# Kernel tuning notes

Hardware: AMD Instinct MI355X
Metric: run time of the kernel (lower is better)

## Reference

```python
import jax, jax.numpy as jnp
import numpy as np

B, L, DI, D, DO = 64, 1024, 256, 256, 256


def setup_inputs() -> dict:
    key = jax.random.key(0)
    ks = jax.random.split(key, 8)
    s = 1.0 / np.sqrt(D)

    def lin(k, din, dout):
        k1, k2 = jax.random.split(k)
        w = jax.random.normal(k1, (din, dout), dtype=jnp.float32) * s
        b = jax.random.normal(k2, (dout,), dtype=jnp.float32) * s
        return w, b

    Wi_w, Wi_b = lin(ks[0], DI, D)
    Wx_w, Wx_b = lin(ks[1], D, D)
    Ux_w, Ux_b = lin(ks[2], D, D)
    Rx_w, Rx_b = lin(ks[3], D, D)
    Wr_w, Wr_b = lin(ks[4], D, D)
    Wu_w, Wu_b = lin(ks[5], D, D)
    Wo_w, Wo_b = lin(ks[6], D, DO)
    inputs = jax.random.normal(ks[7], (B, L, DI), dtype=jnp.float32)
    return dict(inputs=inputs,
                Wi_w=Wi_w, Wi_b=Wi_b, Wx_w=Wx_w, Wx_b=Wx_b,
                Ux_w=Ux_w, Ux_b=Ux_b, Rx_w=Rx_w, Rx_b=Rx_b,
                Wr_w=Wr_w, Wr_b=Wr_b, Wu_w=Wu_w, Wu_b=Wu_b,
                Wo_w=Wo_w, Wo_b=Wo_b)


def reference(inputs, Wi_w, Wi_b, Wx_w, Wx_b, Ux_w, Ux_b, Rx_w, Rx_b,
              Wr_w, Wr_b, Wu_w, Wu_b, Wo_w, Wo_b):
    x = inputs @ Wi_w + Wi_b  # [B, L, D]

    def run(xd):
        # precompute input projections (one big GEMM each)
        x_x = xd @ Wx_w + Wx_b
        x_r = xd @ Ux_w + Ux_b
        x_u = xd @ Rx_w + Rx_b

        def step(h, xs):
            xx, xr, xu = xs
            r = jax.nn.sigmoid(h @ Wr_w + Wr_b + xr)
            u = jax.nn.sigmoid(h @ Wu_w + Wu_b + xu)
            cand = jnp.tanh(r * h + xx)  # note: module applies r to raw h, no extra matmul
            h_new = u * h + (1.0 - u) * cand
            return h_new, h_new

        h0 = jnp.zeros((xd.shape[0], D), dtype=xd.dtype)
        xs = (jnp.swapaxes(x_x, 0, 1), jnp.swapaxes(x_r, 0, 1), jnp.swapaxes(x_u, 0, 1))
        _, out = jax.lax.scan(step, h0, xs)  # out: [L, B, D]
        return jnp.swapaxes(out, 0, 1)

    out = run(x)
    # bi_gru=True: same weights over time-reversed sequence
    out = out + jnp.flip(run(jnp.flip(x, axis=1)), axis=1)
    return out @ Wo_w + Wo_b
```

## Files before the change

### kernel.cpp

```cpp
#include <hip/hip_runtime.h>


typedef float   f32x4 __attribute__((ext_vector_type(4)));
typedef short   s16x8 __attribute__((ext_vector_type(8)));
typedef int     i32x4 __attribute__((ext_vector_type(4)));
typedef unsigned int u32;
typedef unsigned short u16;

#define LDP  264

__device__ __forceinline__ u16 f2bf(float x) {
    u32 u = __float_as_uint(x);
    return (u16)((u + 0x7FFFu + ((u >> 16) & 1u)) >> 16);
}
__device__ __forceinline__ float bflo(u32 u) { return __uint_as_float(u << 16); }
__device__ __forceinline__ float bfhi(u32 u) { return __uint_as_float(u & 0xFFFF0000u); }
__device__ __forceinline__ float bf2f(u16 v) { return __uint_as_float((u32)v << 16); }

__device__ __forceinline__ float sigm(float z) {
    float e = __builtin_amdgcn_exp2f(z * -1.44269504f);
    return __builtin_amdgcn_rcpf(1.0f + e);
}
__device__ __forceinline__ float tanhfast(float y) {
    float e = __builtin_amdgcn_exp2f(y * 2.88539008f);
    return 1.0f - 2.0f * __builtin_amdgcn_rcpf(1.0f + e);
}

__device__ __forceinline__ void bar_lgkm() {
    asm volatile("s_waitcnt lgkmcnt(0)" ::: "memory");
    __builtin_amdgcn_s_barrier();
    asm volatile("" ::: "memory");
}
__device__ __forceinline__ void bar_only() {
    asm volatile("" ::: "memory");
    __builtin_amdgcn_s_barrier();
    asm volatile("" ::: "memory");
}

#define GLD_LDS16(g, l) __builtin_amdgcn_global_load_lds( \
    (const __attribute__((address_space(1))) unsigned int*)(g), \
    (__attribute__((address_space(3))) unsigned int*)(l), 16, 0, 0)

__global__ __launch_bounds__(256, 2)
void gemm256(const void* __restrict__ Asrc, int a_f32, const u16* __restrict__ A2,
             const float* __restrict__ W, const float* __restrict__ b1,
             const float* __restrict__ b2, void* __restrict__ Cdst, int c_f32, int M)
{
    __shared__ u16 At[32 * LDP];
    const int tid  = threadIdx.x;
    const int lane = tid & 63, wv = tid >> 6;
    const int quad = lane >> 4, n16 = lane & 15;

    s16x8 bw[4][8];
    #pragma unroll
    for (int nt = 0; nt < 4; ++nt) {
        const int col = wv * 64 + nt * 16 + n16;
        #pragma unroll
        for (int kt = 0; kt < 8; ++kt) {
            const int kb0 = kt * 32 + quad * 8;
            s16x8 f;
            #pragma unroll
            for (int j = 0; j < 8; ++j) f[j] = (short)f2bf(W[(kb0 + j) * 256 + col]);
            bw[nt][kt] = f;
        }
    }

    const int arow = tid >> 3, kb = (tid & 7) * 32;
    float av[32];
    const int nstrip = M >> 5;
    const int stride = (int)gridDim.x;

    auto load_strip = [&](int ss) __attribute__((always_inline)) {
        const long base = (long)(ss * 32 + arow) * 256 + kb;
        if (a_f32) {
            const float4* p = (const float4*)((const float*)Asrc + base);
            #pragma unroll
            for (int i = 0; i < 8; ++i) {
                float4 v = p[i];
                av[i*4+0] = v.x; av[i*4+1] = v.y; av[i*4+2] = v.z; av[i*4+3] = v.w;
            }
        } else {
            const uint4* p = (const uint4*)((const u16*)Asrc + base);
            #pragma unroll
            for (int i = 0; i < 4; ++i) {
                uint4 v = p[i];
                av[i*8+0] = bflo(v.x); av[i*8+1] = bfhi(v.x);
                av[i*8+2] = bflo(v.y); av[i*8+3] = bfhi(v.y);
                av[i*8+4] = bflo(v.z); av[i*8+5] = bfhi(v.z);
                av[i*8+6] = bflo(v.w); av[i*8+7] = bfhi(v.w);
            }
            if (A2) {
                const uint4* q = (const uint4*)(A2 + base);
                #pragma unroll
                for (int i = 0; i < 4; ++i) {
                    uint4 v = q[i];
                    av[i*8+0] += bflo(v.x); av[i*8+1] += bfhi(v.x);
                    av[i*8+2] += bflo(v.y); av[i*8+3] += bfhi(v.y);
                    av[i*8+4] += bflo(v.z); av[i*8+5] += bfhi(v.z);
                    av[i*8+6] += bflo(v.w); av[i*8+7] += bfhi(v.w);
                }
            }
        }
    };

    int s = (int)blockIdx.x;
    if (s < nstrip) load_strip(s);

    for (; s < nstrip; ) {
        bar_only();
        {
            u16 tmp[32];
            #pragma unroll
            for (int i = 0; i < 32; ++i) tmp[i] = f2bf(av[i]);
            s16x8* dst = (s16x8*)&At[arow * LDP + kb];
            #pragma unroll
            for (int i = 0; i < 4; ++i) dst[i] = *(const s16x8*)&tmp[i * 8];
        }
        bar_lgkm();

        const int snext = s + stride;
        if (snext < nstrip) load_strip(snext);

        f32x4 acc[2][4];
        #pragma unroll
        for (int mt = 0; mt < 2; ++mt)
            #pragma unroll
            for (int nt = 0; nt < 4; ++nt) acc[mt][nt] = f32x4{0.f, 0.f, 0.f, 0.f};
        #pragma unroll
        for (int kt = 0; kt < 8; ++kt) {
            const int ko = kt * 32 + quad * 8;
            const s16x8 a0 = *(const s16x8*)&At[(n16) * LDP + ko];
            const s16x8 a1 = *(const s16x8*)&At[(16 + n16) * LDP + ko];
            #pragma unroll
            for (int nt = 0; nt < 4; ++nt) {
                acc[0][nt] = __builtin_amdgcn_mfma_f32_16x16x32_bf16(a0, bw[nt][kt], acc[0][nt], 0, 0, 0);
                acc[1][nt] = __builtin_amdgcn_mfma_f32_16x16x32_bf16(a1, bw[nt][kt], acc[1][nt], 0, 0, 0);
            }
        }

        #pragma unroll
        for (int nt = 0; nt < 4; ++nt) {
            const int col = wv * 64 + nt * 16 + n16;
            const float bias = b1[col] + (b2 ? b2[col] : 0.0f);
            #pragma unroll
            for (int mt = 0; mt < 2; ++mt) {
                const int row0 = s * 32 + mt * 16 + quad * 4;
                #pragma unroll
                for (int r = 0; r < 4; ++r) {
                    const float v = acc[mt][nt][r] + bias;
                    const long idx = (long)(row0 + r) * 256 + col;
                    if (c_f32) ((float*)Cdst)[idx] = v;
                    else       ((u16*)Cdst)[idx]   = f2bf(v);
                }
            }
        }
        s = snext;
    }
}

__global__ __launch_bounds__(256, 2)
void gemm_p2(const u16* __restrict__ X,
             const float* __restrict__ W0, const float* __restrict__ W1, const float* __restrict__ W2,
             const float* __restrict__ bA0, const float* __restrict__ bA1, const float* __restrict__ bA2,
             const float* __restrict__ bB1, const float* __restrict__ bB2,
             u16* __restrict__ C0, u16* __restrict__ C1, u16* __restrict__ C2)
{
    __shared__ u16 At[2][32 * 256];
    const int tid  = threadIdx.x;
    const int lane = tid & 63, wv = tid >> 6;
    const int quad = lane >> 4, n16 = lane & 15;

    const int m  = (int)blockIdx.x >> 9;
    const int s0 = (int)blockIdx.x & 511;
    const float* W  = (m == 0) ? W0 : ((m == 1) ? W1 : W2);
    const float* b1 = (m == 0) ? bA0 : ((m == 1) ? bA1 : bA2);
    const float* b2 = (m == 0) ? (const float*)nullptr : ((m == 1) ? bB1 : bB2);
    u16* C = (m == 0) ? C0 : ((m == 1) ? C1 : C2);

    s16x8 bw[4][8];
    #pragma unroll
    for (int nt = 0; nt < 4; ++nt) {
        const int col = wv * 64 + nt * 16 + n16;
        #pragma unroll
        for (int kt = 0; kt < 8; ++kt) {
            const int kb0 = kt * 32 + quad * 8;
            s16x8 f;
            #pragma unroll
            for (int j = 0; j < 8; ++j) f[j] = (short)f2bf(W[(kb0 + j) * 256 + col]);
            bw[nt][kt] = f;
        }
    }

    u32 myL[4];
    #pragma unroll
    for (int r = 0; r < 4; ++r) {
        const u32 p = ((u32)(wv * 4 + r) * 64 + (u32)lane) * 16;
        myL[r] = p ^ (((p >> 9) & 7u) << 4);
    }
    const u32 key   = ((u32)(n16 & 7)) << 4;
    const u32 base0 = (u32)n16 * 512 + (u32)quad * 16;
    const u32 base1 = base0 + 16 * 512;

    {
        const char* src = (const char*)(X + (long)s0 * 32 * 256);
        #pragma unroll
        for (int r = 0; r < 4; ++r)
            GLD_LDS16(src + myL[r], (char*)&At[0][0] + (u32)(wv * 4 + r) * 1024);
    }

    int cur = 0;
    for (int s = s0; s < 2048; s += 512) {
        asm volatile("s_waitcnt vmcnt(0)" ::: "memory");
        bar_only();

        const int snext = s + 512;
        if (snext < 2048) {
            const char* src = (const char*)(X + (long)snext * 32 * 256);
            #pragma unroll
            for (int r = 0; r < 4; ++r)
                GLD_LDS16(src + myL[r], (char*)&At[cur ^ 1][0] + (u32)(wv * 4 + r) * 1024);
        }

        const char* atc = (const char*)&At[cur][0];
        f32x4 acc[2][4];
        #pragma unroll
        for (int mt = 0; mt < 2; ++mt)
            #pragma unroll
            for (int nt = 0; nt < 4; ++nt) acc[mt][nt] = f32x4{0.f, 0.f, 0.f, 0.f};
        #pragma unroll
        for (int kt = 0; kt < 8; ++kt) {
            const s16x8 a0 = *(const s16x8*)(atc + (((base0 + (u32)kt * 64) ^ key)));
            const s16x8 a1 = *(const s16x8*)(atc + (((base1 + (u32)kt * 64) ^ key)));
            #pragma unroll
            for (int nt = 0; nt < 4; ++nt) {
                acc[0][nt] = __builtin_amdgcn_mfma_f32_16x16x32_bf16(a0, bw[nt][kt], acc[0][nt], 0, 0, 0);
                acc[1][nt] = __builtin_amdgcn_mfma_f32_16x16x32_bf16(a1, bw[nt][kt], acc[1][nt], 0, 0, 0);
            }
        }

        #pragma unroll
        for (int nt = 0; nt < 4; ++nt) {
            const int col = wv * 64 + nt * 16 + n16;
            const float bias = b1[col] + (b2 ? b2[col] : 0.0f);
            #pragma unroll
            for (int mt = 0; mt < 2; ++mt) {
                const int row0 = s * 32 + mt * 16 + quad * 4;
                #pragma unroll
                for (int r = 0; r < 4; ++r) {
                    const float v = acc[mt][nt][r] + bias;
                    C[(long)(row0 + r) * 256 + col] = f2bf(v);
                }
            }
        }
        cur ^= 1;
    }
}

__global__ __launch_bounds__(512, 2)
void gru_rec(const u16* __restrict__ XX, const u16* __restrict__ XR, const u16* __restrict__ XU,
             const float* __restrict__ Wr, const float* __restrict__ Wu,
             u16* __restrict__ Hf, u16* __restrict__ Hb)
{
    __shared__ __attribute__((aligned(16))) char hb8[2][2 * 320];
    __shared__ float sdq[8][2][32];

    const int tid  = threadIdx.x;
    const int lane = tid & 63, wave = tid >> 6;
    const int quad = lane >> 4, n16 = lane & 15;
    const int wg  = blockIdx.x;
    const int dir = wg >> 5;
    const int b0  = (wg & 31) * 2;
    const int c0  = wave * 32;

    i32x4 aw[2][2][4];
    #pragma unroll
    for (int g = 0; g < 2; ++g) {
        const float* Wg = g ? Wu : Wr;
        #pragma unroll
        for (int nt = 0; nt < 2; ++nt) {
            const int col = c0 + nt * 16 + n16;
            float wv64[64];
            float amax = 0.f;
            #pragma unroll
            for (int kt = 0; kt < 4; ++kt)
                #pragma unroll
                for (int j = 0; j < 16; ++j) {
                    const float w = Wg[(kt * 64 + quad * 16 + j) * 256 + col];
                    wv64[kt * 16 + j] = w;
                    amax = fmaxf(amax, fabsf(w));
                }
            amax = fmaxf(amax, __shfl_xor(amax, 16));
            amax = fmaxf(amax, __shfl_xor(amax, 32));
            const float inv = 127.f / amax;
            #pragma unroll
            for (int kt = 0; kt < 4; ++kt) {
                u32 b[4];
                #pragma unroll
                for (int d = 0; d < 4; ++d) {
                    u32 v = 0;
                    #pragma unroll
                    for (int e = 0; e < 4; ++e) {
                        const int qi = (int)__builtin_rintf(wv64[kt * 16 + d * 4 + e] * inv);
                        v |= ((u32)(qi & 255u)) << (8 * e);
                    }
                    b[d] = v;
                }
                aw[g][nt][kt] = (i32x4){(int)b[0], (int)b[1], (int)b[2], (int)b[3]};
            }
            if (quad == 0) sdq[wave][g][nt * 16 + n16] = amax * (1.0f / 16129.f);
        }
    }

    const int  eseq = lane >> 5;
    const int  ecl  = lane & 31;
    const int  ntb  = ecl >> 4;
    const int  gcol = c0 + ecl;
    const long xrow = (long)(b0 + eseq) * 1024;
    float hprev = 0.0f;

    for (int i = tid; i < 2 * 320; i += 512) hb8[0][i] = 0;

    u16* const Hg = dir ? Hb : Hf;

    u16 cxx, cxr, cxu;
    {
        const long off = (xrow + (dir ? 1023 : 0)) * 256 + gcol;
        cxx = XX[off]; cxr = XR[off]; cxu = XU[off];
    }
    __syncthreads();
    const float srq = sdq[wave][0][ecl];
    const float suq = sdq[wave][1][ecl];

    auto stepbody = [&](int step, int pb) __attribute__((always_inline)) {
        const int t = dir ? 1023 - step : step;
        int sn = step + 1; if (sn > 1023) sn = 1023;
        const int tn = dir ? 1023 - sn : sn;

        const long offn = (xrow + tn) * 256 + gcol;
        const u16 nxx = XX[offn], nxr = XR[offn], nxu = XU[offn];

        const char* hin = &hb8[pb][0] + (n16 & 1) * 320;
        i32x4 a00 = (i32x4){0,0,0,0}, a01 = a00, a10 = a00, a11 = a00;
        #pragma unroll
        for (int kt = 0; kt < 4; ++kt) {
            const i32x4 hv = *(const i32x4*)(hin + kt * 64 + quad * 16);
            a00 = __builtin_amdgcn_mfma_i32_16x16x64_i8(hv, aw[0][0][kt], a00, 0, 0, 0);
            a01 = __builtin_amdgcn_mfma_i32_16x16x64_i8(hv, aw[0][1][kt], a01, 0, 0, 0);
            a10 = __builtin_amdgcn_mfma_i32_16x16x64_i8(hv, aw[1][0][kt], a10, 0, 0, 0);
            a11 = __builtin_amdgcn_mfma_i32_16x16x64_i8(hv, aw[1][1][kt], a11, 0, 0, 0);
        }

        const int pri = ntb ? (eseq ? a01[1] : a01[0]) : (eseq ? a00[1] : a00[0]);
        const int pui = ntb ? (eseq ? a11[1] : a11[0]) : (eseq ? a10[1] : a10[0]);
        const float pr = (float)pri * srq;
        const float pu = (float)pui * suq;

        const float rr   = sigm(pr + bf2f(cxr));
        const float uu   = sigm(pu + bf2f(cxu));
        const float cand = tanhfast(rr * hprev + bf2f(cxx));
        hprev = cand + uu * (hprev - cand);

        hb8[pb ^ 1][eseq * 320 + gcol] = (char)(int)__builtin_rintf(hprev * 127.f);
        Hg[(xrow + t) * 256 + gcol]    = f2bf(hprev);

        cxx = nxx; cxr = nxr; cxu = nxu;
        bar_lgkm();
    };

    for (int sp = 0; sp < 512; ++sp) {
        stepbody(sp * 2,     0);
        stepbody(sp * 2 + 1, 1);
    }
}

extern "C" void kernel_launch(void* const* d_in, const int* in_sizes, int n_in,
                              void* d_out, int out_size, void* d_ws, size_t ws_size,
                              hipStream_t stream)
{
    const float* inputs = (const float*)d_in[0];
    const float* Wi_w = (const float*)d_in[1];
    const float* Wi_b = (const float*)d_in[2];
    const float* Wx_w = (const float*)d_in[3];
    const float* Wx_b = (const float*)d_in[4];
    const float* Ux_w = (const float*)d_in[5];
    const float* Ux_b = (const float*)d_in[6];
    const float* Rx_w = (const float*)d_in[7];
    const float* Rx_b = (const float*)d_in[8];
    const float* Wr_w = (const float*)d_in[9];
    const float* Wr_b = (const float*)d_in[10];
    const float* Wu_w = (const float*)d_in[11];
    const float* Wu_b = (const float*)d_in[12];
    const float* Wo_w = (const float*)d_in[13];
    const float* Wo_b = (const float*)d_in[14];

    const long E = 64L * 1024 * 256;
    u16* XX = (u16*)d_ws;
    u16* XR = XX + E;
    u16* XU = XR + E;
    u16* Hf = XU + E;
    u16* Hb = Hf + E;
    u16* Xb = Hf;

    const int M = 64 * 1024;
    const dim3 gg(512), gb(256);

    hipLaunchKernelGGL(gemm256, gg, gb, 0, stream,
                       (const void*)inputs, 1, (const u16*)nullptr, Wi_w, Wi_b, (const float*)nullptr,
                       (void*)Xb, 0, M);
    hipLaunchKernelGGL(gemm_p2, dim3(1536), gb, 0, stream,
                       (const u16*)Xb,
                       Wx_w, Ux_w, Rx_w,
                       Wx_b, Ux_b, Rx_b,
                       Wr_b, Wu_b,
                       XX, XR, XU);
    hipLaunchKernelGGL(gru_rec, dim3(64), dim3(512), 0, stream,
                       (const u16*)XX, (const u16*)XR, (const u16*)XU, Wr_w, Wu_w, Hf, Hb);
    hipLaunchKernelGGL(gemm256, gg, gb, 0, stream,
                       (const void*)Hf, 0, (const u16*)Hb, Wo_w, Wo_b, (const float*)nullptr,
                       d_out, 1, M);
}
```

Before: 697.0 us.

## Fold input projection into gate weights and fuse output sum into GEMM

Precomputes the combined weights Wi·Wx, Wi·Ux, Wi·Rx and matching biases in a small prep kernel. The three gate projections are then computed directly from the fp32 inputs, which removes the separate input GEMM and its bf16 intermediate round trip. The output GEMM now streams Hf and Hb via direct-to-LDS loads and accumulates both through MFMA, instead of adding them in registers after conversion. The trade-off is that the 1536 gate blocks each reread fp32 inputs, plus a tiny serial prep kernel and slightly different rounding.

Result: slower. 753.9 us (+8.2%).

```diff
diff --git a/kernel.cpp b/kernel.cpp
--- a/kernel.cpp
+++ b/kernel.cpp
@@ -42,15 +42,57 @@
     (__attribute__((address_space(3))) unsigned int*)(l), 16, 0, 0)
 
 __global__ __launch_bounds__(256, 2)
-void gemm256(const void* __restrict__ Asrc, int a_f32, const u16* __restrict__ A2,
-             const float* __restrict__ W, const float* __restrict__ b1,
-             const float* __restrict__ b2, void* __restrict__ Cdst, int c_f32, int M)
+void prep(const float* __restrict__ Wi_w, const float* __restrict__ Wi_b,
+          const float* __restrict__ Wx_w, const float* __restrict__ Wx_b,
+          const float* __restrict__ Ux_w, const float* __restrict__ Ux_b,
+          const float* __restrict__ Rx_w, const float* __restrict__ Rx_b,
+          const float* __restrict__ Wr_b, const float* __restrict__ Wu_b,
+          float* __restrict__ WP, float* __restrict__ BP)
+{
+    const int b = (int)blockIdx.x, n = (int)threadIdx.x;
+    if (b < 24) {
+        const int m = b >> 3, s = b & 7;
+        const float* W = (m == 0) ? Wx_w : ((m == 1) ? Ux_w : Rx_w);
+        float acc[32];
+        #pragma unroll
+        for (int r = 0; r < 32; ++r) acc[r] = 0.f;
+        for (int k = 0; k < 256; ++k) {
+            const float wv = W[k * 256 + n];
+            const float* wi = Wi_w + (s * 32) * 256 + k;
+            #pragma unroll
+            for (int r = 0; r < 32; ++r) acc[r] = fmaf(wi[r * 256], wv, acc[r]);
+        }
+        float* dst = WP + m * 65536 + (s * 32) * 256 + n;
+        #pragma unroll
+        for (int r = 0; r < 32; ++r) dst[r * 256] = acc[r];
+    } else {
+        #pragma unroll
+        for (int m = 0; m < 3; ++m) {
+            const float* W = (m == 0) ? Wx_w : ((m == 1) ? Ux_w : Rx_w);
+            float acc = (m == 0) ? Wx_b[n]
+                      : ((m == 1) ? Ux_b[n] + Wr_b[n] : Rx_b[n] + Wu_b[n]);
+            for (int k = 0; k < 256; ++k) acc = fmaf(Wi_b[k], W[k * 256 + n], acc);
+            BP[m * 256 + n] = acc;
+        }
+    }
+}
+
+__global__ __launch_bounds__(256, 2)
+void gemm_p3(const float* __restrict__ A, const float* __restrict__ WP,
+             const float* __restrict__ BP,
+             u16* __restrict__ C0, u16* __restrict__ C1, u16* __restrict__ C2)
 {
     __shared__ u16 At[32 * LDP];
     const int tid  = threadIdx.x;
     const int lane = tid & 63, wv = tid >> 6;
     const int quad = lane >> 4, n16 = lane & 15;
 
+    const int m  = (int)blockIdx.x >> 9;
+    const int s0 = (int)blockIdx.x & 511;
+    const float* W  = WP + m * 65536;
+    const float* b1 = BP + m * 256;
+    u16* C = (m == 0) ? C0 : ((m == 1) ? C1 : C2);
+
     s16x8 bw[4][8];
     #pragma unroll
     for (int nt = 0; nt < 4; ++nt) {
@@ -67,46 +109,19 @@
 
     const int arow = tid >> 3, kb = (tid & 7) * 32;
     float av[32];
-    const int nstrip = M >> 5;
-    const int stride = (int)gridDim.x;
 
     auto load_strip = [&](int ss) __attribute__((always_inline)) {
-        const long base = (long)(ss * 32 + arow) * 256 + kb;
-        if (a_f32) {
-            const float4* p = (const float4*)((const float*)Asrc + base);
-            #pragma unroll
-            for (int i = 0; i < 8; ++i) {
-                float4 v = p[i];
-                av[i*4+0] = v.x; av[i*4+1] = v.y; av[i*4+2] = v.z; av[i*4+3] = v.w;
-            }
-        } else {
-            const uint4* p = (const uint4*)((const u16*)Asrc + base);
-            #pragma unroll
-            for (int i = 0; i < 4; ++i) {
-                uint4 v = p[i];
-                av[i*8+0] = bflo(v.x); av[i*8+1] = bfhi(v.x);
-                av[i*8+2] = bflo(v.y); av[i*8+3] = bfhi(v.y);
-                av[i*8+4] = bflo(v.z); av[i*8+5] = bfhi(v.z);
-                av[i*8+6] = bflo(v.w); av[i*8+7] = bfhi(v.w);
-            }
-            if (A2) {
-                const uint4* q = (const uint4*)(A2 + base);
-                #pragma unroll
-                for (int i = 0; i < 4; ++i) {
-                    uint4 v = q[i];
-                    av[i*8+0] += bflo(v.x); av[i*8+1] += bfhi(v.x);
-                    av[i*8+2] += bflo(v.y); av[i*8+3] += bfhi(v.y);
-                    av[i*8+4] += bflo(v.z); av[i*8+5] += bfhi(v.z);
-                    av[i*8+6] += bflo(v.w); av[i*8+7] += bfhi(v.w);
-                }
-            }
+        const float4* p = (const float4*)(A + (long)(ss * 32 + arow) * 256 + kb);
+        #pragma unroll
+        for (int i = 0; i < 8; ++i) {
+            float4 v = p[i];
+            av[i*4+0] = v.x; av[i*4+1] = v.y; av[i*4+2] = v.z; av[i*4+3] = v.w;
         }
     };
 
-    int s = (int)blockIdx.x;
-    if (s < nstrip) load_strip(s);
-
-    for (; s < nstrip; ) {
+    load_strip(s0);
+
+    for (int s = s0; s < 2048; ) {
         bar_only();
         {
             u16 tmp[32];
@@ -118,8 +133,8 @@
         }
         bar_lgkm();
 
-        const int snext = s + stride;
-        if (snext < nstrip) load_strip(snext);
+        const int snext = s + 512;
+        if (snext < 2048) load_strip(snext);
 
         f32x4 acc[2][4];
         #pragma unroll
@@ -141,107 +156,7 @@
         #pragma unroll
         for (int nt = 0; nt < 4; ++nt) {
             const int col = wv * 64 + nt * 16 + n16;
-            const float bias = b1[col] + (b2 ? b2[col] : 0.0f);
-            #pragma unroll
-            for (int mt = 0; mt < 2; ++mt) {
-                const int row0 = s * 32 + mt * 16 + quad * 4;
-                #pragma unroll
-                for (int r = 0; r < 4; ++r) {
-                    const float v = acc[mt][nt][r] + bias;
-                    const long idx = (long)(row0 + r) * 256 + col;
-                    if (c_f32) ((float*)Cdst)[idx] = v;
-                    else       ((u16*)Cdst)[idx]   = f2bf(v);
-                }
-            }
-        }
-        s = snext;
-    }
-}
-
-__global__ __launch_bounds__(256, 2)
-void gemm_p2(const u16* __restrict__ X,
-             const float* __restrict__ W0, const float* __restrict__ W1, const float* __restrict__ W2,
-             const float* __restrict__ bA0, const float* __restrict__ bA1, const float* __restrict__ bA2,
-             const float* __restrict__ bB1, const float* __restrict__ bB2,
-             u16* __restrict__ C0, u16* __restrict__ C1, u16* __restrict__ C2)
-{
-    __shared__ u16 At[2][32 * 256];
-    const int tid  = threadIdx.x;
-    const int lane = tid & 63, wv = tid >> 6;
-    const int quad = lane >> 4, n16 = lane & 15;
-
-    const int m  = (int)blockIdx.x >> 9;
-    const int s0 = (int)blockIdx.x & 511;
-    const float* W  = (m == 0) ? W0 : ((m == 1) ? W1 : W2);
-    const float* b1 = (m == 0) ? bA0 : ((m == 1) ? bA1 : bA2);
-    const float* b2 = (m == 0) ? (const float*)nullptr : ((m == 1) ? bB1 : bB2);
-    u16* C = (m == 0) ? C0 : ((m == 1) ? C1 : C2);
-
-    s16x8 bw[4][8];
-    #pragma unroll
-    for (int nt = 0; nt < 4; ++nt) {
-        const int col = wv * 64 + nt * 16 + n16;
-        #pragma unroll
-        for (int kt = 0; kt < 8; ++kt) {
-            const int kb0 = kt * 32 + quad * 8;
-            s16x8 f;
-            #pragma unroll
-            for (int j = 0; j < 8; ++j) f[j] = (short)f2bf(W[(kb0 + j) * 256 + col]);
-            bw[nt][kt] = f;
-        }
-    }
-
-    u32 myL[4];
-    #pragma unroll
-    for (int r = 0; r < 4; ++r) {
-        const u32 p = ((u32)(wv * 4 + r) * 64 + (u32)lane) * 16;
-        myL[r] = p ^ (((p >> 9) & 7u) << 4);
-    }
-    const u32 key   = ((u32)(n16 & 7)) << 4;
-    const u32 base0 = (u32)n16 * 512 + (u32)quad * 16;
-    const u32 base1 = base0 + 16 * 512;
-
-    {
-        const char* src = (const char*)(X + (long)s0 * 32 * 256);
-        #pragma unroll
-        for (int r = 0; r < 4; ++r)
-            GLD_LDS16(src + myL[r], (char*)&At[0][0] + (u32)(wv * 4 + r) * 1024);
-    }
-
-    int cur = 0;
-    for (int s = s0; s < 2048; s += 512) {
-        asm volatile("s_waitcnt vmcnt(0)" ::: "memory");
-        bar_only();
-
-        const int snext = s + 512;
-        if (snext < 2048) {
-            const char* src = (const char*)(X + (long)snext * 32 * 256);
-            #pragma unroll
-            for (int r = 0; r < 4; ++r)
-                GLD_LDS16(src + myL[r], (char*)&At[cur ^ 1][0] + (u32)(wv * 4 + r) * 1024);
-        }
-
-        const char* atc = (const char*)&At[cur][0];
-        f32x4 acc[2][4];
-        #pragma unroll
-        for (int mt = 0; mt < 2; ++mt)
-            #pragma unroll
-            for (int nt = 0; nt < 4; ++nt) acc[mt][nt] = f32x4{0.f, 0.f, 0.f, 0.f};
-        #pragma unroll
-        for (int kt = 0; kt < 8; ++kt) {
-            const s16x8 a0 = *(const s16x8*)(atc + (((base0 + (u32)kt * 64) ^ key)));
-            const s16x8 a1 = *(const s16x8*)(atc + (((base1 + (u32)kt * 64) ^ key)));
-            #pragma unroll
-            for (int nt = 0; nt < 4; ++nt) {
-                acc[0][nt] = __builtin_amdgcn_mfma_f32_16x16x32_bf16(a0, bw[nt][kt], acc[0][nt], 0, 0, 0);
-                acc[1][nt] = __builtin_amdgcn_mfma_f32_16x16x32_bf16(a1, bw[nt][kt], acc[1][nt], 0, 0, 0);
-            }
-        }
-
-        #pragma unroll
-        for (int nt = 0; nt < 4; ++nt) {
-            const int col = wv * 64 + nt * 16 + n16;
-            const float bias = b1[col] + (b2 ? b2[col] : 0.0f);
+            const float bias = b1[col];
             #pragma unroll
             for (int mt = 0; mt < 2; ++mt) {
                 const int row0 = s * 32 + mt * 16 + quad * 4;
@@ -252,7 +167,102 @@
                 }
             }
         }
-        cur ^= 1;
+        s = snext;
+    }
+}
+
+__global__ __launch_bounds__(256, 2)
+void gemm_f(const u16* __restrict__ Hf, const u16* __restrict__ Hb,
+            const float* __restrict__ W, const float* __restrict__ bias,
+            float* __restrict__ out)
+{
+    __shared__ u16 At[2][32 * 256];
+    const int tid  = threadIdx.x;
+    const int lane = tid & 63, wv = tid >> 6;
+    const int quad = lane >> 4, n16 = lane & 15;
+
+    s16x8 bw[4][8];
+    #pragma unroll
+    for (int nt = 0; nt < 4; ++nt) {
+        const int col = wv * 64 + nt * 16 + n16;
+        #pragma unroll
+        for (int kt = 0; kt < 8; ++kt) {
+            const int kb0 = kt * 32 + quad * 8;
+            s16x8 f;
+            #pragma unroll
+            for (int j = 0; j < 8; ++j) f[j] = (short)f2bf(W[(kb0 + j) * 256 + col]);
+            bw[nt][kt] = f;
+        }
+    }
+
+    u32 myL[4];
+    #pragma unroll
+    for (int r = 0; r < 4; ++r) {
+        const u32 p = ((u32)(wv * 4 + r) * 64 + (u32)lane) * 16;
+        myL[r] = p ^ (((p >> 9) & 7u) << 4);
+    }
+    const u32 key   = ((u32)(n16 & 7)) << 4;
+    const u32 base0 = (u32)n16 * 512 + (u32)quad * 16;
+    const u32 base1 = base0 + 16 * 512;
+
+    auto stage = [&](int ss) __attribute__((always_inline)) {
+        const char* f = (const char*)(Hf + (long)ss * 32 * 256);
+        const char* b = (const char*)(Hb + (long)ss * 32 * 256);
+        #pragma unroll
+        for (int r = 0; r < 4; ++r)
+            GLD_LDS16(f + myL[r], (char*)&At[0][0] + (u32)(wv * 4 + r) * 1024);
+        #pragma unroll
+        for (int r = 0; r < 4; ++r)
+            GLD_LDS16(b + myL[r], (char*)&At[1][0] + (u32)(wv * 4 + r) * 1024);
+    };
+
+    const int s0 = (int)blockIdx.x;
+    stage(s0);
+
+    for (int s = s0; s < 2048; s += 512) {
+        asm volatile("s_waitcnt vmcnt(0)" ::: "memory");
+        bar_only();
+
+        const char* atf = (const char*)&At[0][0];
+        const char* atb = (const char*)&At[1][0];
+        f32x4 acc[2][4];
+        #pragma unroll
+        for (int mt = 0; mt < 2; ++mt)
+            #pragma unroll
+            for (int nt = 0; nt < 4; ++nt) acc[mt][nt] = f32x4{0.f, 0.f, 0.f, 0.f};
+        #pragma unroll
+        for (int kt = 0; kt < 8; ++kt) {
+            const s16x8 f0 = *(const s16x8*)(atf + (((base0 + (u32)kt * 64) ^ key)));
+            const s16x8 f1 = *(const s16x8*)(atf + (((base1 + (u32)kt * 64) ^ key)));
+            const s16x8 g0 = *(const s16x8*)(atb + (((base0 + (u32)kt * 64) ^ key)));
+            const s16x8 g1 = *(const s16x8*)(atb + (((base1 + (u32)kt * 64) ^ key)));
+            #pragma unroll
+            for (int nt = 0; nt < 4; ++nt) {
+                acc[0][nt] = __builtin_amdgcn_mfma_f32_16x16x32_bf16(f0, bw[nt][kt], acc[0][nt], 0, 0, 0);
+                acc[1][nt] = __builtin_amdgcn_mfma_f32_16x16x32_bf16(f1, bw[nt][kt], acc[1][nt], 0, 0, 0);
+                acc[0][nt] = __builtin_amdgcn_mfma_f32_16x16x32_bf16(g0, bw[nt][kt], acc[0][nt], 0, 0, 0);
+                acc[1][nt] = __builtin_amdgcn_mfma_f32_16x16x32_bf16(g1, bw[nt][kt], acc[1][nt], 0, 0, 0);
+            }
+        }
+
+        #pragma unroll
+        for (int nt = 0; nt < 4; ++nt) {
+            const int col = wv * 64 + nt * 16 + n16;
+            const float bv = bias[col];
+            #pragma unroll
+            for (int mt = 0; mt < 2; ++mt) {
+                const int row0 = s * 32 + mt * 16 + quad * 4;
+                #pragma unroll
+                for (int r = 0; r < 4; ++r)
+                    out[(long)(row0 + r) * 256 + col] = acc[mt][nt][r] + bv;
+            }
+        }
+
+        const int snext = s + 512;
+        if (snext < 2048) {
+            bar_only();
+            stage(snext);
+        }
     }
 }
 
@@ -399,23 +409,16 @@
     u16* XU = XR + E;
     u16* Hf = XU + E;
     u16* Hb = Hf + E;
-    u16* Xb = Hf;
-
-    const int M = 64 * 1024;
-    const dim3 gg(512), gb(256);
-
-    hipLaunchKernelGGL(gemm256, gg, gb, 0, stream,
-                       (const void*)inputs, 1, (const u16*)nullptr, Wi_w, Wi_b, (const float*)nullptr,
-                       (void*)Xb, 0, M);
-    hipLaunchKernelGGL(gemm_p2, dim3(1536), gb, 0, stream,
-                       (const u16*)Xb,
-                       Wx_w, Ux_w, Rx_w,
-                       Wx_b, Ux_b, Rx_b,
-                       Wr_b, Wu_b,
-                       XX, XR, XU);
+    float* WP = (float*)Hf;
+    float* BP = WP + 3 * 65536;
+
+    hipLaunchKernelGGL(prep, dim3(25), dim3(256), 0, stream,
+                       Wi_w, Wi_b, Wx_w, Wx_b, Ux_w, Ux_b, Rx_w, Rx_b,
+                       Wr_b, Wu_b, WP, BP);
+    hipLaunchKernelGGL(gemm_p3, dim3(1536), dim3(256), 0, stream,
+                       inputs, WP, BP, XX, XR, XU);
     hipLaunchKernelGGL(gru_rec, dim3(64), dim3(512), 0, stream,
                        (const u16*)XX, (const u16*)XR, (const u16*)XU, Wr_w, Wu_w, Hf, Hb);
-    hipLaunchKernelGGL(gemm256, gg, gb, 0, stream,
-                       (const void*)Hf, 0, (const u16*)Hb, Wo_w, Wo_b, (const float*)nullptr,
-                       d_out, 1, M);
-}
+    hipLaunchKernelGGL(gemm_f, dim3(512), dim3(256), 0, stream,
+                       (const u16*)Hf, (const u16*)Hb, Wo_w, Wo_b, (float*)d_out);
+}
```
